# Performance work log

Measured on AMD Instinct MI355X. Metric: run time of the kernel, lower is better.

The kernel has to match this reference:

```python
import jax, jax.numpy as jnp
import numpy as np

N_S = 4096      # number of sentences
N_K = 8192      # number of knowledge entries
HID = 1024      # settings.hidden_dim
SENT = 1024     # settings.sent_dim


def setup_inputs() -> dict:
    key = jax.random.key(0)
    ks = jax.random.split(key, 6)
    sentences = jax.random.normal(ks[0], (N_S, SENT), dtype=jnp.float32)
    knowledge = jax.random.normal(ks[1], (N_K, 3 * HID), dtype=jnp.float32)
    # Linear params stored as [in, out] for x @ W + b
    Ws = jax.random.normal(ks[2], (SENT, HID), dtype=jnp.float32) * 0.02
    bs = jnp.zeros((HID,), dtype=jnp.float32)
    Wk = jax.random.normal(ks[3], (3 * HID, HID), dtype=jnp.float32) * 0.02
    bk = jnp.zeros((HID,), dtype=jnp.float32)
    return {"sentences": sentences, "knowledge": knowledge,
            "Ws": Ws, "bs": bs, "Wk": Wk, "bk": bk}


def reference(sentences, knowledge, Ws, bs, Wk, bk):
    S = sentences @ Ws + bs                  # [N_s, h]
    K = knowledge @ Wk + bk                  # [N_k, h]
    align_scores = S @ K.T                   # [N_s, N_k]
    # NOTE: softmax over dim=0 (sentence axis), exactly as the torch module
    attentions = jax.nn.softmax(align_scores, axis=0)
    fused = attentions @ knowledge           # [N_s, 3h]
    return (fused, attentions)
```

## Files before the change

### kernel.cpp

```cpp
#include <hip/hip_runtime.h>
#include <hip/hip_bf16.h>
#include <cstdint>
#include <cstddef>

#define N_S 4096
#define N_Kn 8192
#define HID 1024
#define SENT 1024
#define K3 3072

typedef __attribute__((ext_vector_type(4))) float f4;
typedef __attribute__((ext_vector_type(8))) short bf8;
typedef __attribute__((ext_vector_type(4))) short bf4;
typedef unsigned short u16;

__device__ __forceinline__ u16 f2bf(float x) {
    __hip_bfloat16 h = __float2bfloat16(x);
    return __builtin_bit_cast(u16, h);
}
__device__ __forceinline__ float bf2f(u16 u) {
    union { unsigned int u; float f; } v; v.u = ((unsigned int)u) << 16;
    return v.f;
}

__device__ __forceinline__ void gl16(const u16* g, u16* l) {
    __builtin_amdgcn_global_load_lds(
        (const __attribute__((address_space(1))) void*)g,
        (__attribute__((address_space(3))) void*)l, 16, 0, 0);
}

__device__ __forceinline__ int xcd_swz(int bid, int nwg) {
    const int cpx = nwg >> 3;
    return (bid & 7) * cpx + (bid >> 3);
}

#define BARR __builtin_amdgcn_s_barrier()
#define PRIO1 __builtin_amdgcn_s_setprio(1)
#define PRIO0 __builtin_amdgcn_s_setprio(0)
#define VM7  asm volatile("s_waitcnt vmcnt(7)" ::: "memory")
#define VM6  asm volatile("s_waitcnt vmcnt(6)" ::: "memory")
#define VM0  asm volatile("s_waitcnt vmcnt(0)" ::: "memory")

__global__ __launch_bounds__(256) void transpose_split_f32(
    const float* __restrict__ in, u16* __restrict__ hi, u16* __restrict__ lo,
    int R, int C)
{
    __shared__ float tile[32][33];
    const int bx = blockIdx.x * 32, by = blockIdx.y * 32;
    const int tx = threadIdx.x & 31, ty = threadIdx.x >> 5;
#pragma unroll
    for (int i = 0; i < 32; i += 8)
        tile[ty + i][tx] = in[(size_t)(by + ty + i) * C + bx + tx];
    __syncthreads();
#pragma unroll
    for (int i = 0; i < 32; i += 8) {
        const float v = tile[tx][ty + i];
        const u16 h = f2bf(v);
        const size_t o = (size_t)(bx + ty + i) * R + by + tx;
        hi[o] = h;
        lo[o] = f2bf(v - bf2f(h));
    }
}

__global__ __launch_bounds__(256) void transpose_f32_bf16(
    const float* __restrict__ in, u16* __restrict__ out, int R, int C)
{
    __shared__ float tile[32][33];
    const int bx = blockIdx.x * 32, by = blockIdx.y * 32;
    const int tx = threadIdx.x & 31, ty = threadIdx.x >> 5;
#pragma unroll
    for (int i = 0; i < 32; i += 8)
        tile[ty + i][tx] = in[(size_t)(by + ty + i) * C + bx + tx];
    __syncthreads();
#pragma unroll
    for (int i = 0; i < 32; i += 8)
        out[(size_t)(bx + ty + i) * R + by + tx] = f2bf(tile[tx][ty + i]);
}

#define GB_LDA(buf, mh) \
  _Pragma("unroll") for (int mf_ = 0; mf_ < 2; ++mf_) \
  _Pragma("unroll") for (int kk_ = 0; kk_ < 2; ++kk_) \
    fa[mf_][kk_] = *(const bf8*)&sA[buf][(wm*64 + ((mh)*2+mf_)*16 + fr)*64 + (((kk_*4+kg) ^ (fr&7))<<3)];

#define GB_LDB(buf, nh, FB) \
  _Pragma("unroll") for (int nf_ = 0; nf_ < 3; ++nf_) \
  _Pragma("unroll") for (int kk_ = 0; kk_ < 2; ++kk_) \
    FB[nf_][kk_] = *(const bf8*)&sB[buf][(wn*96 + ((nh)*3+nf_)*16 + fr)*64 + (((kk_*4+kg) ^ (fr&7))<<3)];

#define GB_MMA(mh, nh, FB) \
  _Pragma("unroll") for (int kk_ = 0; kk_ < 2; ++kk_) \
  _Pragma("unroll") for (int mf_ = 0; mf_ < 2; ++mf_) \
  _Pragma("unroll") for (int nf_ = 0; nf_ < 3; ++nf_) \
    acc[(mh)*2+mf_][(nh)*3+nf_] = __builtin_amdgcn_mfma_f32_16x16x32_bf16( \
        fa[mf_][kk_], FB[nf_][kk_], acc[(mh)*2+mf_][(nh)*3+nf_], 0, 0, 0);

__global__ __launch_bounds__(512, 2) void gemm8b(
    const u16* __restrict__ A, const u16* __restrict__ B,
    float* __restrict__ C, int N, int Kd, int gx)
{
    __shared__ u16 sA[2][256 * 64];
    __shared__ u16 sB[2][192 * 64];

    const int swz = xcd_swz(blockIdx.x, gridDim.x);
    const int bx = swz % gx, by = swz / gx;
    const long brow = (long)by * 256, bcol = (long)bx * 192;

    const int t = threadIdx.x;
    const int w = t >> 6, l = t & 63;
    const int fr = l & 15, kg = l >> 4;
    const int wm = w >> 1;
    const int wn = w & 1;

    const int srow = t >> 3;
    const int schk = ((t & 7) ^ (srow & 7)) << 3;
    const int sldb = w << 9;

    const u16* pA0 = A + (brow +   0 + srow) * (long)Kd + schk;
    const u16* pA1 = A + (brow +  64 + srow) * (long)Kd + schk;
    const u16* pA2 = A + (brow + 128 + srow) * (long)Kd + schk;
    const u16* pA3 = A + (brow + 192 + srow) * (long)Kd + schk;
    const u16* pB0 = B + (bcol +   0 + srow) * (long)Kd + schk;
    const u16* pB1 = B + (bcol +  64 + srow) * (long)Kd + schk;
    const u16* pB2 = B + (bcol + 128 + srow) * (long)Kd + schk;

    auto stB3 = [&](int buf) {
        u16* base = &sB[buf][0];
        gl16(pB0, base + sldb);
        gl16(pB1, base + 4096 + sldb);
        gl16(pB2, base + 8192 + sldb);
    };
    auto stA4 = [&](int buf) {
        u16* base = &sA[buf][0];
        gl16(pA0, base + sldb);
        gl16(pA1, base + 4096 + sldb);
        gl16(pA2, base + 8192 + sldb);
        gl16(pA3, base + 12288 + sldb);
    };
    auto advance = [&]() {
        pA0 += 64; pA1 += 64; pA2 += 64; pA3 += 64;
        pB0 += 64; pB1 += 64; pB2 += 64;
    };

    f4 acc[4][6];
#pragma unroll
    for (int m = 0; m < 4; ++m)
#pragma unroll
        for (int n = 0; n < 6; ++n) acc[m][n] = (f4){0.f, 0.f, 0.f, 0.f};

    bf8 fa[2][2], fb0[3][2], fb1[3][2];

    const int NK = Kd >> 6;

    stB3(0); stA4(0); advance();
    stB3(1); stA4(1); advance();
    VM7;
    BARR;
    GB_LDB(0, 0, fb0);

    for (int kt = 0; kt < NK; ++kt) {
        const int buf = kt & 1;
        const bool s2 = kt + 2 < NK;
        const bool more = kt + 1 < NK;

        GB_LDA(buf, 0);
        BARR; PRIO1; GB_MMA(0, 0, fb0); PRIO0;

        GB_LDB(buf, 1, fb1);
        BARR; PRIO1; GB_MMA(0, 1, fb1); PRIO0;

        GB_LDA(buf, 1);
        if (s2) { stB3(buf); }
        BARR; PRIO1; GB_MMA(1, 0, fb0); PRIO0;

        if (s2) { stA4(buf); VM7; } else { VM0; }
        BARR;
        if (more) { GB_LDB(buf ^ 1, 0, fb0); }
        PRIO1; GB_MMA(1, 1, fb1); PRIO0;
        advance();
    }

#pragma unroll
    for (int n = 0; n < 6; ++n) {
        const long c = bcol + wn * 96 + n * 16 + fr;
#pragma unroll
        for (int m = 0; m < 4; ++m) {
            const long r0 = brow + wm * 64 + m * 16 + kg * 4;
#pragma unroll
            for (int r = 0; r < 4; ++r)
                C[(r0 + r) * (long)N + c] = acc[m][n][r];
        }
    }
}

#define GS_LD(buf) \
  _Pragma("unroll") for (int m_ = 0; m_ < 4; ++m_) { \
    fah[m_] = *(const bf8*)&sAh[buf][(wm*64 + m_*16 + fr)*32 + kq]; \
    fal[m_] = *(const bf8*)&sAl[buf][(wm*64 + m_*16 + fr)*32 + kq]; } \
  _Pragma("unroll") for (int j_ = 0; j_ < 4; ++j_) { \
    fbh[j_] = *(const bf8*)&sBh[buf][(wn*64 + j_*16 + fr)*32 + kq]; \
    fbl[j_] = *(const bf8*)&sBl[buf][(wn*64 + j_*16 + fr)*32 + kq]; }

#define GS_MMA(nlo) \
  _Pragma("unroll") for (int m_ = 0; m_ < 4; ++m_) \
  _Pragma("unroll") for (int j_ = 0; j_ < 2; ++j_) { \
    const int n_ = (nlo)*2 + j_; \
    acc[m_][n_] = __builtin_amdgcn_mfma_f32_16x16x32_bf16(fah[m_], fbh[n_], acc[m_][n_], 0, 0, 0); \
    acc[m_][n_] = __builtin_amdgcn_mfma_f32_16x16x32_bf16(fah[m_], fbl[n_], acc[m_][n_], 0, 0, 0); \
    acc[m_][n_] = __builtin_amdgcn_mfma_f32_16x16x32_bf16(fal[m_], fbh[n_], acc[m_][n_], 0, 0, 0); }

__global__ __launch_bounds__(512, 2) void gemm8s(
    const u16* __restrict__ Ah, const u16* __restrict__ Al,
    const u16* __restrict__ Bh, const u16* __restrict__ Bl,
    float* __restrict__ C, float* __restrict__ pm, float* __restrict__ ps,
    int N, int Kd)
{
    __shared__ u16 sAh[2][8192], sAl[2][8192];
    __shared__ u16 sBh[2][4096], sBl[2][4096];

    const int bid = blockIdx.x;
    const int q = bid >> 3;
    const int by = (bid & 7) * 2 + (q & 1);
    const int bx = q >> 1;
    const long brow = (long)by * 256, bcol = (long)bx * 128;

    const int t = threadIdx.x;
    const int w = t >> 6, l = t & 63;
    const int fr = l & 15, kg = l >> 4;
    const int wm = w >> 1;
    const int wn = w & 1;
    const int kq = (kg ^ ((fr >> 1) & 3)) << 3;

    const int srow = t >> 2;
    const int schk = ((t & 3) ^ ((t >> 3) & 3)) << 3;
    const int sldb = w << 9;

    const u16* pAh0 = Ah + (brow + srow) * (long)Kd + schk;
    const u16* pAh1 = Ah + (brow + 128 + srow) * (long)Kd + schk;
    const u16* pAl0 = Al + (brow + srow) * (long)Kd + schk;
    const u16* pAl1 = Al + (brow + 128 + srow) * (long)Kd + schk;
    const u16* pBh0 = Bh + (bcol + srow) * (long)Kd + schk;
    const u16* pBl0 = Bl + (bcol + srow) * (long)Kd + schk;

    auto stage6 = [&](int buf) {
        gl16(pBh0, &sBh[buf][sldb]);
        gl16(pBl0, &sBl[buf][sldb]);
        gl16(pAh0, &sAh[buf][sldb]);
        gl16(pAh1, &sAh[buf][4096 + sldb]);
        gl16(pAl0, &sAl[buf][sldb]);
        gl16(pAl1, &sAl[buf][4096 + sldb]);
    };
    auto advance = [&]() {
        pAh0 += 32; pAh1 += 32; pAl0 += 32; pAl1 += 32;
        pBh0 += 32; pBl0 += 32;
    };

    f4 acc[4][4];
#pragma unroll
    for (int m = 0; m < 4; ++m)
#pragma unroll
        for (int n = 0; n < 4; ++n) acc[m][n] = (f4){0.f, 0.f, 0.f, 0.f};

    bf8 fah[4], fal[4], fbh[4], fbl[4];

    const int NK = Kd >> 5;

    stage6(0); advance();
    stage6(1); advance();
    VM6;
    BARR;

    for (int kt = 0; kt < NK; ++kt) {
        const int buf = kt & 1;
        const bool s2 = kt + 2 < NK;

        GS_LD(buf);
        BARR; PRIO1; GS_MMA(0); PRIO0;

        if (s2) { stage6(buf); VM6; } else { VM0; }
        BARR;
        PRIO1; GS_MMA(1); PRIO0;
        advance();
    }

#pragma unroll
    for (int n = 0; n < 4; ++n) {
        const long c = bcol + wn * 64 + n * 16 + fr;
#pragma unroll
        for (int m = 0; m < 4; ++m) {
            const long r0 = brow + wm * 64 + m * 16 + kg * 4;
#pragma unroll
            for (int r = 0; r < 4; ++r)
                C[(r0 + r) * (long)N + c] = acc[m][n][r];
        }
    }

    float* red = (float*)&sAh[0][0];
    float lmax[4];
#pragma unroll
    for (int n = 0; n < 4; ++n) {
        float m = -3.4e38f;
#pragma unroll
        for (int mm = 0; mm < 4; ++mm)
#pragma unroll
            for (int r = 0; r < 4; ++r) m = fmaxf(m, acc[mm][n][r]);
        m = fmaxf(m, __shfl_xor(m, 16, 64));
        m = fmaxf(m, __shfl_xor(m, 32, 64));
        lmax[n] = m;
    }
    BARR;
    if (kg == 0) {
#pragma unroll
        for (int n = 0; n < 4; ++n)
            red[wm * 128 + wn * 64 + n * 16 + fr] = lmax[n];
    }
    BARR;
    float bmax[4];
#pragma unroll
    for (int n = 0; n < 4; ++n) {
        const int c = wn * 64 + n * 16 + fr;
        bmax[n] = fmaxf(fmaxf(red[c], red[128 + c]),
                        fmaxf(red[256 + c], red[384 + c]));
    }
    BARR;
    float lsum[4];
#pragma unroll
    for (int n = 0; n < 4; ++n) {
        float s = 0.f;
#pragma unroll
        for (int mm = 0; mm < 4; ++mm)
#pragma unroll
            for (int r = 0; r < 4; ++r) s += __expf(acc[mm][n][r] - bmax[n]);
        s += __shfl_xor(s, 16, 64);
        s += __shfl_xor(s, 32, 64);
        lsum[n] = s;
    }
    if (kg == 0) {
#pragma unroll
        for (int n = 0; n < 4; ++n)
            red[wm * 128 + wn * 64 + n * 16 + fr] = lsum[n];
    }
    BARR;
    if (wm == 0 && kg == 0) {
#pragma unroll
        for (int n = 0; n < 4; ++n) {
            const int c = wn * 64 + n * 16 + fr;
            const float bs = red[c] + red[128 + c] + red[256 + c] + red[384 + c];
            pm[(size_t)by * N + bcol + c] = bmax[n];
            ps[(size_t)by * N + bcol + c] = bs;
        }
    }
}

template <bool SPLIT, bool AF32, bool EPIS>
__global__ __launch_bounds__(256) void gemm_mfma(
    const void* __restrict__ Aany, const u16* __restrict__ Alo_,
    const u16* __restrict__ Bhi_, const u16* __restrict__ Blo_,
    float* __restrict__ Cf, u16* __restrict__ Chi, u16* __restrict__ Clo,
    const float* __restrict__ bias, int N, int Kd, int gx)
{
    constexpr int SA = AF32 ? 48 : 32;
    __shared__ u16 sAh[128 * SA];
    __shared__ u16 sAl[SPLIT ? 128 * SA : 8];
    __shared__ u16 sBh[128 * 32];
    __shared__ u16 sBl[SPLIT ? 128 * 32 : 8];

    const int swz = xcd_swz(blockIdx.x, gridDim.x);
    const int nst_x = gx >> 2;
    const int st = swz >> 4, off = swz & 15;
    const int bxi = (st % nst_x) * 4 + (off & 3);
    const int byi = (st / nst_x) * 4 + (off >> 2);

    const int t = threadIdx.x;
    const int w = t >> 6;
    const int l = t & 63;
    const long brow = (long)byi * 128;
    const long bcol = (long)bxi * 128;

    const int grow = l >> 2;
    const int gcol = ((l & 3) ^ ((l >> 3) & 3)) * 8;

    const int wr = (w >> 1) * 64;
    const int wc = (w & 1) * 64;
    const int fr = l & 15;
    const int kg = l >> 4;
    const int kq = (kg ^ ((fr >> 1) & 3)) * 8;

    f4 acc[4][4];
#pragma unroll
    for (int m = 0; m < 4; m++)
#pragma unroll
        for (int n = 0; n < 4; n++) acc[m][n] = (f4){0.f, 0.f, 0.f, 0.f};

    const int nkt = Kd >> 5;
    for (int kt = 0; kt < nkt; ++kt) {
        const int k0 = kt * 32;

#pragma unroll
        for (int i = 0; i < 2; ++i) {
            const long r = bcol + i * 64 + w * 16 + grow;
            const int lb = i * 2048 + w * 512;
            gl16(Bhi_ + r * Kd + k0 + gcol, sBh + lb);
            if constexpr (SPLIT) gl16(Blo_ + r * Kd + k0 + gcol, sBl + lb);
        }

        if constexpr (!AF32) {
            const u16* Ahi = (const u16*)Aany;
#pragma unroll
            for (int i = 0; i < 2; ++i) {
                const long r = brow + i * 64 + w * 16 + grow;
                const int lb = i * 2048 + w * 512;
                gl16(Ahi + r * Kd + k0 + gcol, sAh + lb);
                if constexpr (SPLIT) gl16(Alo_ + r * Kd + k0 + gcol, sAl + lb);
            }
        } else {
            const float* Af = (const float*)Aany;
            const int ar = w * 8 + (l >> 3);
            const int cF = (l & 7) * 4;
#pragma unroll
            for (int j = 0; j < 4; ++j) {
                const int r = j * 32 + ar;
                const f4 v = *(const f4*)(Af + (brow + r) * (long)Kd + k0 + cF);
                u16 h[4], lw[4];
#pragma unroll
                for (int q = 0; q < 4; ++q) {
                    h[q] = f2bf(v[q]);
                    if constexpr (SPLIT) lw[q] = f2bf(v[q] - bf2f(h[q]));
                }
                *(bf4*)&sAh[r * SA + cF] = *(bf4*)h;
                if constexpr (SPLIT) *(bf4*)&sAl[r * SA + cF] = *(bf4*)lw;
            }
        }
        __syncthreads();

        bf8 fah[4], fbh[4], fal[4], fbl[4];
#pragma unroll
        for (int m = 0; m < 4; ++m) {
            if constexpr (AF32) {
                fah[m] = *(bf8*)&sAh[(wr + m * 16 + fr) * SA + kg * 8];
                if constexpr (SPLIT) fal[m] = *(bf8*)&sAl[(wr + m * 16 + fr) * SA + kg * 8];
            } else {
                fah[m] = *(bf8*)&sAh[(wr + m * 16 + fr) * 32 + kq];
                if constexpr (SPLIT) fal[m] = *(bf8*)&sAl[(wr + m * 16 + fr) * 32 + kq];
            }
            fbh[m] = *(bf8*)&sBh[(wc + m * 16 + fr) * 32 + kq];
            if constexpr (SPLIT) fbl[m] = *(bf8*)&sBl[(wc + m * 16 + fr) * 32 + kq];
        }
#pragma unroll
        for (int m = 0; m < 4; ++m)
#pragma unroll
            for (int n = 0; n < 4; ++n) {
                acc[m][n] = __builtin_amdgcn_mfma_f32_16x16x32_bf16(fah[m], fbh[n], acc[m][n], 0, 0, 0);
                if constexpr (SPLIT) {
                    acc[m][n] = __builtin_amdgcn_mfma_f32_16x16x32_bf16(fah[m], fbl[n], acc[m][n], 0, 0, 0);
                    acc[m][n] = __builtin_amdgcn_mfma_f32_16x16x32_bf16(fal[m], fbh[n], acc[m][n], 0, 0, 0);
                }
            }
        __syncthreads();
    }

#pragma unroll
    for (int n = 0; n < 4; ++n) {
        const long c = bcol + wc + n * 16 + fr;
        float bv = 0.f;
        if constexpr (EPIS) bv = bias[c];
#pragma unroll
        for (int m = 0; m < 4; ++m) {
            const long r0 = brow + wr + m * 16 + kg * 4;
#pragma unroll
            for (int r = 0; r < 4; ++r) {
                const float v = acc[m][n][r] + bv;
                if constexpr (EPIS) {
                    const u16 h = f2bf(v);
                    Chi[(r0 + r) * (long)N + c] = h;
                    Clo[(r0 + r) * (long)N + c] = f2bf(v - bf2f(h));
                } else {
                    Cf[(r0 + r) * (long)N + c] = v;
                }
            }
        }
    }
}

#define RCHUNK 128

__global__ __launch_bounds__(256) void softmax_combine(
    const float* __restrict__ pm, const float* __restrict__ ps,
    float* __restrict__ fm, float* __restrict__ fsinv)
{
    const int col = blockIdx.x * 256 + threadIdx.x;
    float m = -3.4e38f;
#pragma unroll
    for (int i = 0; i < 16; i++) m = fmaxf(m, pm[(size_t)i * N_Kn + col]);
    float s = 0.f;
#pragma unroll
    for (int i = 0; i < 16; i++)
        s += ps[(size_t)i * N_Kn + col] * __expf(pm[(size_t)i * N_Kn + col] - m);
    fm[col] = m;
    fsinv[col] = 1.f / s;
}

__global__ __launch_bounds__(256) void softmax_norm(
    float* __restrict__ align, u16* __restrict__ abf,
    const float* __restrict__ fm, const float* __restrict__ fsinv)
{
    const int col = blockIdx.x * 256 + threadIdx.x;
    const int r0 = blockIdx.y * RCHUNK;
    const float m = fm[col], si = fsinv[col];
    for (int r = 0; r < RCHUNK; r++) {
        const size_t idx = (size_t)(r0 + r) * N_Kn + col;
        const float v = __expf(align[idx] - m) * si;
        align[idx] = v;
        abf[idx] = f2bf(v);
    }
}

extern "C" void kernel_launch(void* const* d_in, const int* in_sizes, int n_in,
                              void* d_out, int out_size, void* d_ws, size_t ws_size,
                              hipStream_t stream)
{
    const float* sentences = (const float*)d_in[0];
    const float* knowledge = (const float*)d_in[1];
    const float* Ws = (const float*)d_in[2];
    const float* bs = (const float*)d_in[3];
    const float* Wk = (const float*)d_in[4];
    const float* bk = (const float*)d_in[5];

    float* out_fused = (float*)d_out;
    float* out_attn = (float*)d_out + (size_t)N_S * K3;

    char* w = (char*)d_ws;
    u16* attn_bf = (u16*)w;
    u16* WsT_hi = (u16*)w; w += (size_t)HID * SENT * 2;
    u16* WsT_lo = (u16*)w; w += (size_t)HID * SENT * 2;
    u16* WkT_hi = (u16*)w; w += (size_t)HID * K3 * 2;
    u16* WkT_lo = (u16*)w; w += (size_t)HID * K3 * 2;
    u16* S_hi   = (u16*)w; w += (size_t)N_S * HID * 2;
    u16* S_lo   = (u16*)w; w += (size_t)N_S * HID * 2;
    u16* K_hi   = (u16*)w; w += (size_t)N_Kn * HID * 2;
    u16* K_lo   = (u16*)w; w += (size_t)N_Kn * HID * 2;
    u16* kT     = (u16*)w; w += (size_t)K3 * N_Kn * 2;
    float* pm   = (float*)w; w += (size_t)16 * N_Kn * 4;
    float* ps   = (float*)w; w += (size_t)16 * N_Kn * 4;
    float* fm   = (float*)w; w += (size_t)N_Kn * 4;
    float* fsv  = (float*)w; w += (size_t)N_Kn * 4;

    transpose_split_f32<<<dim3(HID / 32, SENT / 32), 256, 0, stream>>>(Ws, WsT_hi, WsT_lo, SENT, HID);
    transpose_split_f32<<<dim3(HID / 32, K3 / 32), 256, 0, stream>>>(Wk, WkT_hi, WkT_lo, K3, HID);
    transpose_f32_bf16<<<dim3(K3 / 32, N_Kn / 32), 256, 0, stream>>>(knowledge, kT, N_Kn, K3);

    gemm_mfma<true, true, true><<<(HID / 128) * (N_S / 128), 256, 0, stream>>>(
        sentences, nullptr, WsT_hi, WsT_lo, nullptr, S_hi, S_lo, bs, HID, SENT, HID / 128);

    gemm_mfma<true, true, true><<<(HID / 128) * (N_Kn / 128), 256, 0, stream>>>(
        knowledge, nullptr, WkT_hi, WkT_lo, nullptr, K_hi, K_lo, bk, HID, K3, HID / 128);

    gemm8s<<<(N_Kn / 128) * (N_S / 256), 512, 0, stream>>>(
        S_hi, S_lo, K_hi, K_lo, out_attn, pm, ps, N_Kn, HID);

    softmax_combine<<<dim3(N_Kn / 256), 256, 0, stream>>>(pm, ps, fm, fsv);
    softmax_norm<<<dim3(N_Kn / 256, N_S / RCHUNK), 256, 0, stream>>>(out_attn, attn_bf, fm, fsv);

    gemm8b<<<(K3 / 192) * (N_S / 256), 512, 0, stream>>>(
        attn_bf, kT, out_fused, K3, N_Kn, K3 / 192);
}
```

Measured before the change: 691.0 us.

## Add double-buffered 256x128 split-bf16 GEMM for knowledge projection

Replaces the generic gemm_mfma kernel for the knowledge @ Wk projection with a dedicated 512-thread kernel that uses a 256x128 output tile. It double-buffers shared memory, prefetches fp32 A tiles into registers and converts them to hi/lo bf16 while the MFMAs on the previous tile run. B tiles are loaded asynchronously with global_load_lds, synchronised with explicit vmcnt/lgkmcnt waits. This aims to hide global load latency and raise per-block reuse, at the cost of more LDS and registers, which may limit occupancy. It also relies on GS_LD/GS_MMA macros presumably defined elsewhere.

```diff
diff --git a/kernel.cpp b/kernel.cpp
--- a/kernel.cpp
+++ b/kernel.cpp
@@ -37,9 +37,12 @@
 #define BARR __builtin_amdgcn_s_barrier()
 #define PRIO1 __builtin_amdgcn_s_setprio(1)
 #define PRIO0 __builtin_amdgcn_s_setprio(0)
+#define VM8  asm volatile("s_waitcnt vmcnt(8)" ::: "memory")
 #define VM7  asm volatile("s_waitcnt vmcnt(7)" ::: "memory")
 #define VM6  asm volatile("s_waitcnt vmcnt(6)" ::: "memory")
+#define VM2  asm volatile("s_waitcnt vmcnt(2)" ::: "memory")
 #define VM0  asm volatile("s_waitcnt vmcnt(0)" ::: "memory")
+#define LGKM0 asm volatile("s_waitcnt lgkmcnt(0)" ::: "memory")
 
 __global__ __launch_bounds__(256) void transpose_split_f32(
     const float* __restrict__ in, u16* __restrict__ hi, u16* __restrict__ lo,
@@ -351,6 +354,123 @@
     }
 }
 
+__global__ __launch_bounds__(512, 2) void gemm8f(
+    const float* __restrict__ Af, const u16* __restrict__ Bh, const u16* __restrict__ Bl,
+    u16* __restrict__ Chi, u16* __restrict__ Clo, const float* __restrict__ bias,
+    int N, int Kd)
+{
+    __shared__ u16 sAh[2][8192], sAl[2][8192];
+    __shared__ u16 sBh[2][4096], sBl[2][4096];
+
+    const int bid = blockIdx.x;
+    const int q = bid >> 3;
+    const int by = ((bid & 7) << 2) | (q & 3);
+    const int bx = q >> 2;
+    const long brow = (long)by * 256, bcol = (long)bx * 128;
+
+    const int t = threadIdx.x;
+    const int w = t >> 6, l = t & 63;
+    const int fr = l & 15, kg = l >> 4;
+    const int wm = w >> 1;
+    const int wn = w & 1;
+    const int kq = (kg ^ ((fr >> 1) & 3)) << 3;
+
+    const int srow = t >> 2;
+    const int schk = ((t & 3) ^ ((t >> 3) & 3)) << 3;
+    const int sldb = w << 9;
+    const u16* pBh0 = Bh + (bcol + srow) * (long)Kd + schk;
+    const u16* pBl0 = Bl + (bcol + srow) * (long)Kd + schk;
+
+    const float* pA0 = Af + (brow + srow) * (long)Kd + (t & 3) * 8;
+    const float* pA1 = Af + (brow + 128 + srow) * (long)Kd + (t & 3) * 8;
+    const int adst = srow * 32 + schk;
+
+    auto cvt_write = [&](int buf, int dst, const f4& x0, const f4& x1) {
+        float xv[8];
+        *(f4*)&xv[0] = x0; *(f4*)&xv[4] = x1;
+        u16 h[8], lw[8];
+#pragma unroll
+        for (int j = 0; j < 8; ++j) {
+            h[j] = f2bf(xv[j]);
+            lw[j] = f2bf(xv[j] - bf2f(h[j]));
+        }
+        *(bf8*)&sAh[buf][dst] = *(bf8*)h;
+        *(bf8*)&sAl[buf][dst] = *(bf8*)lw;
+    };
+
+    f4 acc[4][4];
+#pragma unroll
+    for (int m = 0; m < 4; ++m)
+#pragma unroll
+        for (int n = 0; n < 4; ++n) acc[m][n] = (f4){0.f, 0.f, 0.f, 0.f};
+
+    bf8 fah[4], fal[4], fbh[4], fbl[4];
+
+    const int NK = Kd >> 5;
+
+    {
+        f4 a00 = *(const f4*)(pA0);      f4 a01 = *(const f4*)(pA0 + 4);
+        f4 a10 = *(const f4*)(pA1);      f4 a11 = *(const f4*)(pA1 + 4);
+        gl16(pBh0, &sBh[0][sldb]); gl16(pBl0, &sBl[0][sldb]);
+        f4 b00 = *(const f4*)(pA0 + 32); f4 b01 = *(const f4*)(pA0 + 36);
+        f4 b10 = *(const f4*)(pA1 + 32); f4 b11 = *(const f4*)(pA1 + 36);
+        gl16(pBh0 + 32, &sBh[1][sldb]); gl16(pBl0 + 32, &sBl[1][sldb]);
+        VM8;
+        cvt_write(0, adst, a00, a01);
+        cvt_write(0, adst + 4096, a10, a11);
+        VM2;
+        cvt_write(1, adst, b00, b01);
+        cvt_write(1, adst + 4096, b10, b11);
+        LGKM0;
+        BARR;
+        pA0 += 64; pA1 += 64; pBh0 += 64; pBl0 += 64;
+    }
+
+    for (int kt = 0; kt < NK; ++kt) {
+        const int buf = kt & 1;
+        const bool s2 = kt + 2 < NK;
+
+        GS_LD(buf);
+        f4 x0, x1, y0, y1;
+        if (s2) {
+            x0 = *(const f4*)(pA0); x1 = *(const f4*)(pA0 + 4);
+            y0 = *(const f4*)(pA1); y1 = *(const f4*)(pA1 + 4);
+        }
+        BARR; PRIO1; GS_MMA(0); PRIO0;
+
+        if (s2) {
+            gl16(pBh0, &sBh[buf][sldb]);
+            gl16(pBl0, &sBl[buf][sldb]);
+            VM2;
+            cvt_write(buf, adst, x0, x1);
+            cvt_write(buf, adst + 4096, y0, y1);
+            LGKM0;
+        } else {
+            VM0;
+        }
+        BARR;
+        PRIO1; GS_MMA(1); PRIO0;
+        pA0 += 32; pA1 += 32; pBh0 += 32; pBl0 += 32;
+    }
+
+#pragma unroll
+    for (int n = 0; n < 4; ++n) {
+        const long c = bcol + wn * 64 + n * 16 + fr;
+        const float bv = bias[c];
+#pragma unroll
+        for (int m = 0; m < 4; ++m) {
+            const long r0 = brow + wm * 64 + m * 16 + kg * 4;
+#pragma unroll
+            for (int r = 0; r < 4; ++r) {
+                const float v = acc[m][n][r] + bv;
+                const u16 h = f2bf(v);
+                Chi[(r0 + r) * (long)N + c] = h;
+                Clo[(r0 + r) * (long)N + c] = f2bf(v - bf2f(h));
+            }
+        }
+    }
+}
+
 template <bool SPLIT, bool AF32, bool EPIS>
 __global__ __launch_bounds__(256) void gemm_mfma(
     const void* __restrict__ Aany, const u16* __restrict__ Alo_,
@@ -422,9 +542,9 @@
                 const f4 v = *(const f4*)(Af + (brow + r) * (long)Kd + k0 + cF);
                 u16 h[4], lw[4];
 #pragma unroll
-                for (int q = 0; q < 4; ++q) {
-                    h[q] = f2bf(v[q]);
-                    if constexpr (SPLIT) lw[q] = f2bf(v[q] - bf2f(h[q]));
+                for (int qq = 0; qq < 4; ++qq) {
+                    h[qq] = f2bf(v[qq]);
+                    if constexpr (SPLIT) lw[qq] = f2bf(v[qq] - bf2f(h[qq]));
                 }
                 *(bf4*)&sAh[r * SA + cF] = *(bf4*)h;
                 if constexpr (SPLIT) *(bf4*)&sAl[r * SA + cF] = *(bf4*)lw;
@@ -551,8 +671,8 @@
     gemm_mfma<true, true, true><<<(HID / 128) * (N_S / 128), 256, 0, stream>>>(
         sentences, nullptr, WsT_hi, WsT_lo, nullptr, S_hi, S_lo, bs, HID, SENT, HID / 128);
 
-    gemm_mfma<true, true, true><<<(HID / 128) * (N_Kn / 128), 256, 0, stream>>>(
-        knowledge, nullptr, WkT_hi, WkT_lo, nullptr, K_hi, K_lo, bk, HID, K3, HID / 128);
+    gemm8f<<<256, 512, 0, stream>>>(
+        knowledge, WkT_hi, WkT_lo, K_hi, K_lo, bk, HID, K3);
 
     gemm8s<<<(N_Kn / 128) * (N_S / 256), 512, 0, stream>>>(
         S_hi, S_lo, K_hi, K_lo, out_attn, pm, ps, N_Kn, HID);
```

Result: no change. 679.5 us (-1.7%).
